# Kernel tuning notes

Hardware: AMD Instinct MI355X
Metric: run time of the kernel (lower is better)

The kernel has to match this reference:

```python
import jax, jax.numpy as jnp
import numpy as np

# Window-batch of 16x16 windows from a U-Net stage
B, C, H, W = 128, 128, 16, 16
HEADS = 8
EQK, EV = 128, 512      # embed_dim_qk, embed_dim_v (embed_dim=512, ratio=4)
L = H * W               # tokens per window (stride=1)


def _conv3x3(x, w, b):
    # NCHW 3x3 conv, padding 1
    out = jax.lax.conv_general_dilated(x, w, (1, 1), ((1, 1), (1, 1)),
                                       dimension_numbers=('NCHW', 'OIHW', 'NCHW'))
    return out + b[None, :, None, None]


def _pos_att(q, wq, bq, wk, bk, wv, bv, wo, bo, gamma):
    # MultiHeadAttention2D_POS, stride=1 -> conv_q/k/v are 1x1 convs
    hd, hdv = EQK // HEADS, EV // HEADS

    def proj(x, w, bias, d):
        y = jnp.einsum('bchw,ec->behw', x, w) + bias[None, :, None, None]
        return y.reshape(B, HEADS, d, L).transpose(0, 1, 3, 2)  # (B,h,L,d)

    pq = proj(q, wq, bq, hd)
    pk = proj(q, wk, bk, hd)
    pv = proj(q, wv, bv, hdv)
    attn = jax.nn.softmax(jnp.einsum('bhqd,bhkd->bhqk', pq, pk) * hd ** -0.5, axis=-1)
    out = jnp.einsum('bhqk,bhkd->bhqd', attn, pv)
    out = out.transpose(0, 1, 3, 2).reshape(B, EV, H, W)
    out = _conv3x3(out, wo, bo)             # proj_out: 3x3 conv EV->C
    return q + out * gamma                  # gamma-scaled residual


def _cha_att(q, wq, bq, wk, bk, wv, bv, wo, bo, gamma):
    # MultiHeadAttention2D_CHA: depthwise 1x1 grouped convs (channel multiplier = HEADS),
    # attention over the CHANNEL axis. Faithfully reproduces torch's reshape of the
    # group-major (c*HEADS+h) channel layout into (B, heads, C, L).
    def dwproj(x, w, bias):
        y = (x[:, :, None] * w.reshape(C, HEADS)[None, :, :, None, None]
             + bias.reshape(C, HEADS)[None, :, :, None, None])
        return y.reshape(B, C * HEADS, H, W).reshape(B, HEADS, C, L)

    pq = dwproj(q, wq, bq)
    pk = dwproj(q, wk, bk)
    pv = dwproj(q, wv, bv)
    attn = jax.nn.softmax(jnp.einsum('bhcl,bhdl->bhcd', pq, pk) * L ** -0.5, axis=-1)
    out = jnp.einsum('bhcd,bhdl->bhcl', attn, pv)      # (B,h,C,L)
    out = out.reshape(B, HEADS * C, H, W)
    # proj_out: grouped 1x1 ConvTranspose (== grouped 1x1 conv): sum each HEADS-sized group
    out = (out.reshape(B, C, HEADS, H, W)
           * wo.reshape(C, HEADS)[None, :, :, None, None]).sum(2) + bo[None, :, None, None]
    return q + out * gamma


def _forward(qkv_pos, qkv_cha,
             pos_wq, pos_bq, pos_wk, pos_bk, pos_wv, pos_bv, pos_wo, pos_bo, gamma_pos,
             cha_wq, cha_bq, cha_wk, cha_bk, cha_wv, cha_bv, cha_wo, cha_bo, gamma_cha,
             fuse_w, fuse_b):
    out_pos = _pos_att(qkv_pos, pos_wq, pos_bq, pos_wk, pos_bk, pos_wv, pos_bv,
                       pos_wo, pos_bo, gamma_pos)
    out_cha = _cha_att(qkv_cha, cha_wq, cha_bq, cha_wk, cha_bk, cha_wv, cha_bv,
                       cha_wo, cha_bo, gamma_cha)
    out = (out_pos + out_cha) * 0.5          # att_fusion='add' (slides=0 -> full slices)
    return _conv3x3(out, fuse_w, fuse_b)     # conv_out (Dropout2d is identity at eval)


def setup_inputs() -> dict:
    key = jax.random.key(0)
    ks = jax.random.split(key, 24)
    n = lambda k, shape, s=0.05: jax.random.normal(k, shape, dtype=jnp.float32) * s
    return {
        'qkv_pos': jax.random.normal(ks[0], (B, C, H, W), jnp.float32),
        'qkv_cha': jax.random.normal(ks[1], (B, C, H, W), jnp.float32),
        'pos_wq': n(ks[2], (EQK, C)), 'pos_bq': n(ks[3], (EQK,)),
        'pos_wk': n(ks[4], (EQK, C)), 'pos_bk': n(ks[5], (EQK,)),
        'pos_wv': n(ks[6], (EV, C)), 'pos_bv': n(ks[7], (EV,)),
        'pos_wo': n(ks[8], (C, EV, 3, 3)), 'pos_bo': n(ks[9], (C,)),
        'gamma_pos': jnp.array(0.1, jnp.float32),
        'cha_wq': n(ks[10], (C * HEADS,)), 'cha_bq': n(ks[11], (C * HEADS,)),
        'cha_wk': n(ks[12], (C * HEADS,)), 'cha_bk': n(ks[13], (C * HEADS,)),
        'cha_wv': n(ks[14], (C * HEADS,)), 'cha_bv': n(ks[15], (C * HEADS,)),
        'cha_wo': n(ks[16], (C * HEADS,)), 'cha_bo': n(ks[17], (C,)),
        'gamma_cha': jnp.array(0.1, jnp.float32),
        'fuse_w': n(ks[18], (C, C, 3, 3)), 'fuse_b': n(ks[19], (C,)),
    }


def reference(qkv_pos, qkv_cha,
              pos_wq, pos_bq, pos_wk, pos_bk, pos_wv, pos_bv, pos_wo, pos_bo, gamma_pos,
              cha_wq, cha_bq, cha_wk, cha_bk, cha_wv, cha_bv, cha_wo, cha_bo, gamma_cha,
              fuse_w, fuse_b):
    return _forward(qkv_pos, qkv_cha,
                    pos_wq, pos_bq, pos_wk, pos_bk, pos_wv, pos_bv, pos_wo, pos_bo, gamma_pos,
                    cha_wq, cha_bq, cha_wk, cha_bk, cha_wv, cha_bv, cha_wo, cha_bo, gamma_cha,
                    fuse_w, fuse_b)
```

## Files before the change

### kernel.cpp

```cpp
#include <hip/hip_runtime.h>
#include <cstdint>
#include <cstddef>

typedef unsigned short ushort_t;
typedef unsigned int uint_t;
typedef __attribute__((ext_vector_type(8))) short bf16x8;
typedef __attribute__((ext_vector_type(4))) float f32x4;

#define NB 128
#define NC 128
#define NL 256
#define NH 8
#define HD 16
#define HDV 64
#define NEV 512
#define PHALF 4194304

__device__ __forceinline__ ushort_t f2bf(float f) {
    uint_t u = __float_as_uint(f);
    u += 0x7fffu + ((u >> 16) & 1u);
    return (ushort_t)(u >> 16);
}
__device__ __forceinline__ float bf2f(ushort_t s) {
    return __uint_as_float(((uint_t)s) << 16);
}
__device__ __forceinline__ uint_t pack2(float lo, float hi) {
    uint_t r;
    asm("v_cvt_pk_bf16_f32 %0, %1, %2" : "=v"(r) : "v"(lo), "v"(hi));
    return r;
}

template<int CIN>
__global__ __launch_bounds__(256) void k_wpack(const float* __restrict__ w,
                                               short* __restrict__ wp) {
    int idx = blockIdx.x * 256 + threadIdx.x;
    if (idx >= CIN * 1152) return;
    int j    = idx & 7;
    int lane = (idx >> 3) & 63;
    int frag = idx >> 9;
    int rt   = frag & 7;
    int tap  = (frag >> 3) % 9;
    int ch   = frag / 72;
    int co   = rt * 16 + (lane & 15);
    int g    = lane >> 4;
    int ci   = ch * 32 + g * 8 + j;
    wp[idx] = (short)f2bf(w[((size_t)co * CIN + ci) * 9 + tap]);
}

template<int E>
__global__ __launch_bounds__(256) void k_wpack_qkv(const float* __restrict__ w,
                                                   short* __restrict__ wp) {
    int idx = blockIdx.x * 256 + threadIdx.x;
    if (idx >= E * 128) return;
    int j    = idx & 7;
    int lane = (idx >> 3) & 63;
    int ch   = (idx >> 9) & 3;
    int rt   = idx >> 11;
    int n = lane & 15, g = lane >> 4;
    wp[idx] = (short)f2bf(w[(size_t)(rt*16 + n)*128 + ch*32 + g*8 + j]);
}

__global__ __launch_bounds__(256) void k_xpose(const float* __restrict__ x,
                                               ushort_t* __restrict__ xbf) {
    const int half = blockIdx.x, b = blockIdx.y, t = threadIdx.x;
    const float* src = x + (size_t)b*NC*NL + (size_t)half*64*NL + t;
    uint_t* dst = (uint_t*)(xbf + ((size_t)b*NL + t)*NC + half*64);
    #pragma unroll
    for (int k8 = 0; k8 < 8; ++k8) {
        uint4 u;
        u.x = pack2(src[(k8*8+0)*NL], src[(k8*8+1)*NL]);
        u.y = pack2(src[(k8*8+2)*NL], src[(k8*8+3)*NL]);
        u.z = pack2(src[(k8*8+4)*NL], src[(k8*8+5)*NL]);
        u.w = pack2(src[(k8*8+6)*NL], src[(k8*8+7)*NL]);
        *(uint4*)(dst + k8*4) = u;
    }
}

__global__ __launch_bounds__(512, 4) void k_pos_mfma(
    const ushort_t* __restrict__ xbf,
    const short* __restrict__ wpq, const short* __restrict__ wpk,
    const short* __restrict__ wpv,
    const float* __restrict__ bq, const float* __restrict__ bk,
    const float* __restrict__ bv,
    ushort_t* __restrict__ att)
{
    const int h = blockIdx.x, b = blockIdx.y;
    const int t = threadIdx.x;
    const int lane = t & 63, w = t >> 6;
    const int n = lane & 15, g = lane >> 4;

    __shared__ __align__(16) short lds[26112];

    const f32x4 z4 = {0.f, 0.f, 0.f, 0.f};
    f32x4 qacc[2], kacc[2], vacc[4][2];
    #pragma unroll
    for (int ct = 0; ct < 2; ++ct) { qacc[ct] = z4; kacc[ct] = z4; }
    #pragma unroll
    for (int vt = 0; vt < 4; ++vt)
        #pragma unroll
        for (int ct = 0; ct < 2; ++ct) vacc[vt][ct] = z4;

    const ushort_t* xr = xbf + ((size_t)(b*NL + w*32 + n))*NC;

    #pragma unroll 2
    for (int ch = 0; ch < 4; ++ch) {
        bf16x8 xb[2];
        #pragma unroll
        for (int ct = 0; ct < 2; ++ct)
            xb[ct] = *(const bf16x8*)(xr + ct*16*NC + ch*32 + g*8);
        const size_t fo = ((size_t)((h*4 + ch)*64) + lane) * 8;
        {
            bf16x8 aq = *(const bf16x8*)(wpq + fo);
            #pragma unroll
            for (int ct = 0; ct < 2; ++ct)
                qacc[ct] = __builtin_amdgcn_mfma_f32_16x16x32_bf16(aq, xb[ct], qacc[ct], 0, 0, 0);
        }
        {
            bf16x8 ak = *(const bf16x8*)(wpk + fo);
            #pragma unroll
            for (int ct = 0; ct < 2; ++ct)
                kacc[ct] = __builtin_amdgcn_mfma_f32_16x16x32_bf16(ak, xb[ct], kacc[ct], 0, 0, 0);
        }
        #pragma unroll
        for (int vt = 0; vt < 4; ++vt) {
            bf16x8 av = *(const bf16x8*)(wpv + ((size_t)((((h*4 + vt)*4) + ch)*64) + lane) * 8);
            #pragma unroll
            for (int ct = 0; ct < 2; ++ct)
                vacc[vt][ct] = __builtin_amdgcn_mfma_f32_16x16x32_bf16(xb[ct], av, vacc[vt][ct], 0, 0, 0);
        }
    }

    uint_t qu01[2], qu23[2];
    {
        float bqv[4], bkv[4];
        #pragma unroll
        for (int r = 0; r < 4; ++r) {
            bqv[r] = bq[h*16 + g*4 + r];
            bkv[r] = bk[h*16 + g*4 + r];
        }
        #pragma unroll
        for (int ct = 0; ct < 2; ++ct) {
            qu01[ct] = pack2(qacc[ct][0] + bqv[0], qacc[ct][1] + bqv[1]);
            qu23[ct] = pack2(qacc[ct][2] + bqv[2], qacc[ct][3] + bqv[3]);
            uint2 kp;
            kp.x = pack2(kacc[ct][0] + bkv[0], kacc[ct][1] + bkv[1]);
            kp.y = pack2(kacc[ct][2] + bkv[2], kacc[ct][3] + bkv[3]);
            *(uint2*)&lds[(w*32 + ct*16 + n)*16 + g*4] = kp;
        }
        #pragma unroll
        for (int vt = 0; vt < 4; ++vt) {
            const float bvv = bv[h*64 + vt*16 + n];
            #pragma unroll
            for (int ct = 0; ct < 2; ++ct) {
                uint2 vp;
                vp.x = pack2(vacc[vt][ct][0] + bvv, vacc[vt][ct][1] + bvv);
                vp.y = pack2(vacc[vt][ct][2] + bvv, vacc[vt][ct][3] + bvv);
                *(uint2*)&lds[9216 + (vt*16 + n)*264 + w*32 + ct*16 + g*4] = vp;
            }
        }
    }
    __syncthreads();

    const int a0 = (n + 32*(g & 1)) * 4;
    #pragma unroll 1
    for (int qt = 0; qt < 2; ++qt) {
        union { uint_t u[4]; bf16x8 v; } qfu;
        qfu.u[0] = (uint_t)__builtin_amdgcn_ds_bpermute(a0,      (int)qu01[qt]);
        qfu.u[1] = (uint_t)__builtin_amdgcn_ds_bpermute(a0,      (int)qu23[qt]);
        qfu.u[2] = (uint_t)__builtin_amdgcn_ds_bpermute(a0 + 64, (int)qu01[qt]);
        qfu.u[3] = (uint_t)__builtin_amdgcn_ds_bpermute(a0 + 64, (int)qu23[qt]);
        if (g >= 2) { qfu.u[0] = 0; qfu.u[1] = 0; qfu.u[2] = 0; qfu.u[3] = 0; }
        bf16x8 qf = qfu.v;

        f32x4 s[16];
        #pragma unroll
        for (int kt = 0; kt < 16; ++kt) {
            bf16x8 kf = (bf16x8){0,0,0,0,0,0,0,0};
            if (g < 2) kf = *(const bf16x8*)&lds[(kt*16 + n)*16 + g*8];
            s[kt] = __builtin_amdgcn_mfma_f32_16x16x32_bf16(kf, qf, z4, 0, 0, 0);
        }
        float d0 = 0.f, d1 = 0.f, d2 = 0.f, d3 = 0.f;
        #pragma unroll
        for (int kt = 0; kt < 16; ++kt) {
            float e0 = exp2f(s[kt][0] * 0.36067376022224085f);
            float e1 = exp2f(s[kt][1] * 0.36067376022224085f);
            float e2 = exp2f(s[kt][2] * 0.36067376022224085f);
            float e3 = exp2f(s[kt][3] * 0.36067376022224085f);
            s[kt][0] = e0; s[kt][1] = e1; s[kt][2] = e2; s[kt][3] = e3;
            d0 += e0; d1 += e1; d2 += e2; d3 += e3;
        }
        float den = (d0 + d1) + (d2 + d3);
        den += __shfl_xor(den, 16);
        den += __shfl_xor(den, 32);
        const float inv = 1.f / den;

        f32x4 oacc[4] = {z4, z4, z4, z4};
        #pragma unroll
        for (int c2 = 0; c2 < 8; ++c2) {
            #pragma unroll
            for (int u = 0; u < 2; ++u) {
                const int kt = 2*c2 + u;
                uint2 pp;
                pp.x = pack2(s[kt][0], s[kt][1]);
                pp.y = pack2(s[kt][2], s[kt][3]);
                *(uint2*)&lds[4096 + w*640 + n*40 + u*16 + g*4] = pp;
            }
            bf16x8 pf = *(const bf16x8*)&lds[4096 + w*640 + n*40 + g*8];
            #pragma unroll
            for (int vt = 0; vt < 4; ++vt) {
                bf16x8 av = *(const bf16x8*)&lds[9216 + (vt*16 + n)*264 + c2*32 + g*8];
                oacc[vt] = __builtin_amdgcn_mfma_f32_16x16x32_bf16(av, pf, oacc[vt], 0, 0, 0);
            }
        }
        ushort_t* ap = att + (((size_t)b*NL + (w*32 + qt*16 + n))*NEV + h*HDV + g*4);
        #pragma unroll
        for (int vt = 0; vt < 4; ++vt) {
            uint2 op;
            op.x = pack2(oacc[vt][0]*inv, oacc[vt][1]*inv);
            op.y = pack2(oacc[vt][2]*inv, oacc[vt][3]*inv);
            *(uint2*)(ap + vt*16) = op;
        }
    }
}

__global__ __launch_bounds__(256, 1) void k_conv_ci(
    const ushort_t* __restrict__ att, const short* __restrict__ wp,
    ushort_t* __restrict__ P)
{
    const int kc = blockIdx.x, b = blockIdx.y;
    const int t = threadIdx.x;
    const int lane = t & 63, w = t >> 6;
    const int wr = w >> 1, wc = w & 1;
    const int n = lane & 15, gl = lane >> 4;

    __shared__ __align__(16) short ims[2][10368];

    {
        bf16x8 z = {0,0,0,0,0,0,0,0};
        bf16x8* p = (bf16x8*)&ims[0][0];
        for (int i = t; i < 2592; i += 256) p[i] = z;
    }

    f32x4 acc[4][8];
    #pragma unroll
    for (int i = 0; i < 4; ++i)
        #pragma unroll
        for (int j = 0; j < 8; ++j) acc[i][j] = (f32x4){0.f,0.f,0.f,0.f};

    const ushort_t* abase = att + (size_t)b*NL*NEV + kc*256;
    int soff[4], slots[4];
    #pragma unroll
    for (int i = 0; i < 4; ++i) {
        int id = t + 256*i;
        int gg = id & 3, xx = (id >> 2) & 15, yy = id >> 6;
        soff[i]  = (yy*16 + xx)*NEV + gg*8;
        slots[i] = (((yy+1)*4 + gg)*18 + xx + 1) * 8;
    }

    bf16x8 pre[4];
    #pragma unroll
    for (int i = 0; i < 4; ++i) pre[i] = *(const bf16x8*)(abase + soff[i]);
    __syncthreads();

    const int ybase = wc * 8;
    #pragma unroll 1
    for (int ch = 0; ch < 8; ++ch) {
        short* buf = &ims[ch & 1][0];
        #pragma unroll
        for (int i = 0; i < 4; ++i) *(bf16x8*)&buf[slots[i]] = pre[i];
        if (ch < 7) {
            #pragma unroll
            for (int i = 0; i < 4; ++i)
                pre[i] = *(const bf16x8*)(abase + soff[i] + (ch + 1)*32);
        }
        __syncthreads();
        #pragma unroll
        for (int dx = 0; dx < 3; ++dx) {
            bf16x8 Brow[10];
            #pragma unroll
            for (int r = 0; r < 10; ++r)
                Brow[r] = *(const bf16x8*)&buf[(((ybase + r)*4 + gl)*18 + n + dx) * 8];
            #pragma unroll
            for (int dy = 0; dy < 3; ++dy) {
                bf16x8 Af[4];
                #pragma unroll
                for (int rt = 0; rt < 4; ++rt)
                    Af[rt] = *(const bf16x8*)(wp +
                        ((size_t)(((kc*8 + ch)*9 + dy*3 + dx)*8 + wr*4 + rt)) * 512 + lane*8);
                #pragma unroll
                for (int ct = 0; ct < 8; ++ct)
                    #pragma unroll
                    for (int rt = 0; rt < 4; ++rt)
                        acc[rt][ct] = __builtin_amdgcn_mfma_f32_16x16x32_bf16(
                            Af[rt], Brow[ct + dy], acc[rt][ct], 0, 0, 0);
            }
        }
    }

    ushort_t* Pb = P + (size_t)kc * PHALF + (size_t)b * NL * NC;
    #pragma unroll
    for (int rt = 0; rt < 4; ++rt) {
        const int co0 = wr*64 + rt*16 + gl*4;
        #pragma unroll
        for (int ct = 0; ct < 8; ++ct) {
            const int l = wc*128 + ct*16 + n;
            uint2 u;
            u.x = pack2(acc[rt][ct][0], acc[rt][ct][1]);
            u.y = pack2(acc[rt][ct][2], acc[rt][ct][3]);
            *(uint2*)(Pb + (size_t)l*NC + co0) = u;
        }
    }
}

__global__ __launch_bounds__(256, 1) void k_conv_co(
    const float* __restrict__ comb, const short* __restrict__ wp,
    const float* __restrict__ bias, float* __restrict__ out)
{
    const int coh = blockIdx.x, b = blockIdx.y;
    const int t = threadIdx.x;
    const int lane = t & 63, w = t >> 6;
    const int wr = w >> 1, wc = w & 1;
    const int n = lane & 15, gl = lane >> 4;

    __shared__ __align__(16) short ims[2][10368];

    {
        bf16x8 z = {0,0,0,0,0,0,0,0};
        bf16x8* p = (bf16x8*)&ims[0][0];
        for (int i = t; i < 2592; i += 256) p[i] = z;
    }

    f32x4 acc[2][8];
    #pragma unroll
    for (int i = 0; i < 2; ++i)
        #pragma unroll
        for (int j = 0; j < 8; ++j) acc[i][j] = (f32x4){0.f,0.f,0.f,0.f};

    const float* cbase = comb + (size_t)b*NL*NC;
    int soff[4], slots[4];
    #pragma unroll
    for (int i = 0; i < 4; ++i) {
        int id = t + 256*i;
        int gg = id & 3, xx = (id >> 2) & 15, yy = id >> 6;
        soff[i]  = (yy*16 + xx)*NC + gg*8;
        slots[i] = (((yy+1)*4 + gg)*18 + xx + 1) * 8;
    }

    float4 pa[4], pb[4];
    #pragma unroll
    for (int i = 0; i < 4; ++i) {
        pa[i] = *(const float4*)(cbase + soff[i]);
        pb[i] = *(const float4*)(cbase + soff[i] + 4);
    }
    __syncthreads();

    const int ybase = wc * 8;
    #pragma unroll 1
    for (int ch = 0; ch < 4; ++ch) {
        short* buf = &ims[ch & 1][0];
        #pragma unroll
        for (int i = 0; i < 4; ++i) {
            uint4 u;
            u.x = pack2(pa[i].x, pa[i].y);  u.y = pack2(pa[i].z, pa[i].w);
            u.z = pack2(pb[i].x, pb[i].y);  u.w = pack2(pb[i].z, pb[i].w);
            *(uint4*)&buf[slots[i]] = u;
        }
        if (ch < 3) {
            #pragma unroll
            for (int i = 0; i < 4; ++i) {
                pa[i] = *(const float4*)(cbase + soff[i] + (ch + 1)*32);
                pb[i] = *(const float4*)(cbase + soff[i] + (ch + 1)*32 + 4);
            }
        }
        __syncthreads();
        #pragma unroll
        for (int dx = 0; dx < 3; ++dx) {
            bf16x8 Brow[10];
            #pragma unroll
            for (int r = 0; r < 10; ++r)
                Brow[r] = *(const bf16x8*)&buf[(((ybase + r)*4 + gl)*18 + n + dx) * 8];
            #pragma unroll
            for (int dy = 0; dy < 3; ++dy) {
                bf16x8 Af[2];
                #pragma unroll
                for (int rt = 0; rt < 2; ++rt)
                    Af[rt] = *(const bf16x8*)(wp +
                        ((size_t)((ch*9 + dy*3 + dx)*8 + coh*4 + wr*2 + rt)) * 512 + lane*8);
                #pragma unroll
                for (int ct = 0; ct < 8; ++ct)
                    #pragma unroll
                    for (int rt = 0; rt < 2; ++rt)
                        acc[rt][ct] = __builtin_amdgcn_mfma_f32_16x16x32_bf16(
                            Af[rt], Brow[ct + dy], acc[rt][ct], 0, 0, 0);
            }
        }
    }

    #pragma unroll
    for (int rt = 0; rt < 2; ++rt) {
        const int co0 = coh*64 + wr*32 + rt*16 + gl*4;
        const float c0 = bias[co0+0], c1 = bias[co0+1],
                    c2 = bias[co0+2], c3 = bias[co0+3];
        #pragma unroll
        for (int ct = 0; ct < 8; ++ct) {
            const int l = wc*128 + ct*16 + n;
            f32x4 a = acc[rt][ct];
            out[((size_t)b*NC + co0+0)*NL + l] = c0 + a[0];
            out[((size_t)b*NC + co0+1)*NL + l] = c1 + a[1];
            out[((size_t)b*NC + co0+2)*NL + l] = c2 + a[2];
            out[((size_t)b*NC + co0+3)*NL + l] = c3 + a[3];
        }
    }
}

#define NLP 260
__global__ __launch_bounds__(256) void k_cha(
    const float* __restrict__ xc,
    const float* __restrict__ cwq, const float* __restrict__ cbq,
    const float* __restrict__ cwk, const float* __restrict__ cbk,
    const float* __restrict__ cwv, const float* __restrict__ cbv,
    const float* __restrict__ cwo, const float* __restrict__ cbo,
    const float* __restrict__ gamma,
    const ushort_t* __restrict__ P, const float* __restrict__ qpos,
    const float* __restrict__ pbo, const float* __restrict__ gpos,
    float* __restrict__ comb)
{
    const int h = blockIdx.x, b = blockIdx.y, t = threadIdx.x;
    __shared__ float qh[16][NLP];
    __shared__ float G_s[16][17];
    __shared__ float S_s[16];
    __shared__ float wq_s[128], bq_s[128], wk_s[128], bk_s[128], wv_s[128], bv_s[128];
    __shared__ float A_s[128][17];
    __shared__ float B_s[128];
    __shared__ float M_s[16][17];
    __shared__ float c_s[16];

    #pragma unroll
    for (int j = 0; j < 16; ++j)
        qh[j][t] = xc[((size_t)b*NC + h*16 + j)*NL + t];
    if (t < 128) {
        const int k = h*128 + t;
        wq_s[t] = cwq[k]; bq_s[t] = cbq[k];
        wk_s[t] = cwk[k]; bk_s[t] = cbk[k];
        wv_s[t] = cwv[k]; bv_s[t] = cbv[k];
    }
    __syncthreads();
    {
        const int i = t >> 4, j = t & 15;
        const float4* qi = (const float4*)qh[i];
        const float4* qj = (const float4*)qh[j];
        float gg = 0.f;
        for (int l4 = 0; l4 < NL/4; ++l4) {
            float4 a = qi[l4], c = qj[l4];
            gg = fmaf(a.x,c.x,fmaf(a.y,c.y,fmaf(a.z,c.z,fmaf(a.w,c.w,gg))));
        }
        G_s[i][j] = gg;
    }
    if (t < 16) {
        const float4* qi = (const float4*)qh[t];
        float s = 0.f;
        for (int l4 = 0; l4 < NL/4; ++l4) { float4 a = qi[l4]; s += a.x + a.y + a.z + a.w; }
        S_s[t] = s;
    }
    __syncthreads();
    if (t < 128) {
        const int c2 = t, cg = c2 >> 3;
        const float wqc = wq_s[c2], bqc = bq_s[c2];
        float Pv[16];
        #pragma unroll
        for (int j = 0; j < 16; ++j) Pv[j] = wqc*G_s[cg][j] + bqc*S_s[j];
        const float Qc = wqc*S_s[cg] + bqc*256.0f;
        float mx = -3.0e38f;
        #pragma unroll
        for (int dg = 0; dg < 16; ++dg) {
            #pragma unroll
            for (int dj = 0; dj < 8; ++dj) {
                const int d = dg*8 + dj;
                float s = wk_s[d]*Pv[dg] + bk_s[d]*Qc;
                mx = fmaxf(mx, s);
            }
        }
        float A[16];
        #pragma unroll
        for (int j = 0; j < 16; ++j) A[j] = 0.f;
        float Bv = 0.f, den = 0.f;
        #pragma unroll
        for (int dg = 0; dg < 16; ++dg) {
            #pragma unroll
            for (int dj = 0; dj < 8; ++dj) {
                const int d = dg*8 + dj;
                float s = wk_s[d]*Pv[dg] + bk_s[d]*Qc;
                float e = __expf((s - mx) * 0.0625f);
                den += e;
                A[dg] = fmaf(e, wv_s[d], A[dg]);
                Bv = fmaf(e, bv_s[d], Bv);
            }
        }
        const float inv = 1.f / den;
        #pragma unroll
        for (int j = 0; j < 16; ++j) A_s[c2][j] = A[j]*inv;
        B_s[c2] = Bv*inv;
    }
    __syncthreads();
    {
        const int cl = t >> 4, j = t & 15;
        const int cp = h*16 + cl;
        float m = 0.f;
        #pragma unroll
        for (int hp = 0; hp < 8; ++hp)
            m = fmaf(cwo[cp*8+hp], A_s[cl*8+hp][j], m);
        M_s[cl][j] = m;
        if (j == 0) {
            float cc = cbo[cp];
            #pragma unroll
            for (int hp = 0; hp < 8; ++hp)
                cc = fmaf(cwo[cp*8+hp], B_s[cl*8+hp], cc);
            c_s[cl] = cc;
        }
    }
    __syncthreads();
    {
        const float g  = gamma[0];
        const float gp = gpos[0];
        const int l = t;
        float av[16];
        #pragma unroll
        for (int cl = 0; cl < 16; ++cl) {
            float a = c_s[cl];
            #pragma unroll
            for (int j = 0; j < 16; ++j)
                a = fmaf(M_s[cl][j], qh[j][l], a);
            av[cl] = a;
        }
        const ushort_t* p0 = P + ((size_t)b*NL + l)*NC + h*16;
        const ushort_t* p1 = p0 + PHALF;
        const float* qp = qpos + ((size_t)b*NC + h*16)*NL + l;
        float4* cp4 = (float4*)(comb + ((size_t)b*NL + l)*NC + h*16);
        #pragma unroll
        for (int q = 0; q < 4; ++q) {
            uint2 u0 = *(const uint2*)(p0 + 4*q);
            uint2 u1 = *(const uint2*)(p1 + 4*q);
            float s0 = bf2f((ushort_t)(u0.x & 0xffffu)) + bf2f((ushort_t)(u1.x & 0xffffu));
            float s1 = bf2f((ushort_t)(u0.x >> 16))     + bf2f((ushort_t)(u1.x >> 16));
            float s2 = bf2f((ushort_t)(u0.y & 0xffffu)) + bf2f((ushort_t)(u1.y & 0xffffu));
            float s3 = bf2f((ushort_t)(u0.y >> 16))     + bf2f((ushort_t)(u1.y >> 16));
            float4 c;
            c.x = 0.5f*(qp[(4*q+0)*NL] + gp*(pbo[h*16+4*q+0] + s0) + qh[4*q+0][l] + g*av[4*q+0]);
            c.y = 0.5f*(qp[(4*q+1)*NL] + gp*(pbo[h*16+4*q+1] + s1) + qh[4*q+1][l] + g*av[4*q+1]);
            c.z = 0.5f*(qp[(4*q+2)*NL] + gp*(pbo[h*16+4*q+2] + s2) + qh[4*q+2][l] + g*av[4*q+2]);
            c.w = 0.5f*(qp[(4*q+3)*NL] + gp*(pbo[h*16+4*q+3] + s3) + qh[4*q+3][l] + g*av[4*q+3]);
            cp4[q] = c;
        }
    }
}

extern "C" void kernel_launch(void* const* d_in, const int* in_sizes, int n_in,
                              void* d_out, int out_size, void* d_ws, size_t ws_size,
                              hipStream_t stream)
{
    const float* qpos = (const float*)d_in[0];
    const float* qcha = (const float*)d_in[1];
    const float* pwq  = (const float*)d_in[2];
    const float* pbq  = (const float*)d_in[3];
    const float* pwk  = (const float*)d_in[4];
    const float* pbk  = (const float*)d_in[5];
    const float* pwv  = (const float*)d_in[6];
    const float* pbv  = (const float*)d_in[7];
    const float* pwo  = (const float*)d_in[8];
    const float* pbo  = (const float*)d_in[9];
    const float* gpos = (const float*)d_in[10];
    const float* cwq  = (const float*)d_in[11];
    const float* cbq  = (const float*)d_in[12];
    const float* cwk  = (const float*)d_in[13];
    const float* cbk  = (const float*)d_in[14];
    const float* cwv  = (const float*)d_in[15];
    const float* cbv  = (const float*)d_in[16];
    const float* cwo  = (const float*)d_in[17];
    const float* cbo  = (const float*)d_in[18];
    const float* gcha = (const float*)d_in[19];
    const float* fw   = (const float*)d_in[20];
    const float* fb   = (const float*)d_in[21];
    float* outp = (float*)d_out;

    char* ws = (char*)d_ws;
    ushort_t* att  = (ushort_t*)ws;
    float*    comb = (float*)ws;
    ushort_t* P    = (ushort_t*)(ws + 33554432);
    ushort_t* xbf  = (ushort_t*)(ws + 33554432);
    short*    wp1  = (short*)(ws + 50331648);
    short*    wp2  = (short*)(ws + 51511296);
    short*    wpq  = (short*)(ws + 51806208);
    short*    wpk  = (short*)(ws + 51838976);
    short*    wpv  = (short*)(ws + 51871744);

    k_wpack<NEV><<<dim3((NEV*1152 + 255)/256), 256, 0, stream>>>(pwo, wp1);
    k_wpack<NC ><<<dim3((NC *1152 + 255)/256), 256, 0, stream>>>(fw,  wp2);
    k_wpack_qkv<128><<<dim3(64),  256, 0, stream>>>(pwq, wpq);
    k_wpack_qkv<128><<<dim3(64),  256, 0, stream>>>(pwk, wpk);
    k_wpack_qkv<512><<<dim3(256), 256, 0, stream>>>(pwv, wpv);

    k_xpose<<<dim3(2, NB), 256, 0, stream>>>(qpos, xbf);
    k_pos_mfma<<<dim3(NH, NB), 512, 0, stream>>>(xbf, wpq, wpk, wpv,
                                                 pbq, pbk, pbv, att);
    k_conv_ci<<<dim3(2, NB), 256, 0, stream>>>(att, wp1, P);
    k_cha<<<dim3(NH, NB), 256, 0, stream>>>(qcha, cwq, cbq, cwk, cbk, cwv, cbv,
                                            cwo, cbo, gcha,
                                            P, qpos, pbo, gpos, comb);
    k_conv_co<<<dim3(2, NB), 256, 0, stream>>>(comb, wp2, fb, outp);
}
```

Baseline: 178.4 us.

## Drop LDS im2col staging in 3x3 convs, load B fragments directly from global

Both 3x3 conv kernels stop staging a padded image in LDS and instead gather B fragments straight from global memory with boundary masking. Each block now covers half (or a quarter) of the spatial tile, which doubles the grid and raises the occupancy hint to 4 blocks per CU. The weight pack layout is reordered so each lane reads four contiguous A fragments per tap. The combined intermediate is stored as bf16 instead of fp32, halving that round trip. In exchange the kernels re-read overlapping activations from global/L2 per tap, and precision of the fuse-conv input drops.

Measured after the change: 283.9 us. +59.2%, slower.

```diff
diff --git a/kernel.cpp b/kernel.cpp
--- a/kernel.cpp
+++ b/kernel.cpp
@@ -36,14 +36,14 @@
     int idx = blockIdx.x * 256 + threadIdx.x;
     if (idx >= CIN * 1152) return;
     int j    = idx & 7;
-    int lane = (idx >> 3) & 63;
-    int frag = idx >> 9;
-    int rt   = frag & 7;
-    int tap  = (frag >> 3) % 9;
-    int ch   = frag / 72;
-    int co   = rt * 16 + (lane & 15);
-    int g    = lane >> 4;
-    int ci   = ch * 32 + g * 8 + j;
+    int r    = (idx >> 3) & 3;
+    int lane = (idx >> 5) & 63;
+    int gidx = (idx >> 11) & 1;
+    int tc   = idx >> 12;
+    int tap  = tc % 9;
+    int ch   = tc / 9;
+    int co   = (gidx * 4 + r) * 16 + (lane & 15);
+    int ci   = ch * 32 + (lane >> 4) * 8 + j;
     wp[idx] = (short)f2bf(w[((size_t)co * CIN + ci) * 9 + tap]);
 }
 
@@ -223,76 +223,55 @@
     }
 }
 
-__global__ __launch_bounds__(256, 1) void k_conv_ci(
+__global__ __launch_bounds__(256, 4) void k_conv_ci(
     const ushort_t* __restrict__ att, const short* __restrict__ wp,
     ushort_t* __restrict__ P)
 {
-    const int kc = blockIdx.x, b = blockIdx.y;
+    const int kc = blockIdx.x >> 1, lh = blockIdx.x & 1, b = blockIdx.y;
     const int t = threadIdx.x;
     const int lane = t & 63, w = t >> 6;
     const int wr = w >> 1, wc = w & 1;
     const int n = lane & 15, gl = lane >> 4;
-
-    __shared__ __align__(16) short ims[2][10368];
-
-    {
-        bf16x8 z = {0,0,0,0,0,0,0,0};
-        bf16x8* p = (bf16x8*)&ims[0][0];
-        for (int i = t; i < 2592; i += 256) p[i] = z;
-    }
-
-    f32x4 acc[4][8];
+    const int ybase = lh*8 + wc*4;
+
+    f32x4 acc[4][4];
     #pragma unroll
     for (int i = 0; i < 4; ++i)
         #pragma unroll
-        for (int j = 0; j < 8; ++j) acc[i][j] = (f32x4){0.f,0.f,0.f,0.f};
-
-    const ushort_t* abase = att + (size_t)b*NL*NEV + kc*256;
-    int soff[4], slots[4];
-    #pragma unroll
-    for (int i = 0; i < 4; ++i) {
-        int id = t + 256*i;
-        int gg = id & 3, xx = (id >> 2) & 15, yy = id >> 6;
-        soff[i]  = (yy*16 + xx)*NEV + gg*8;
-        slots[i] = (((yy+1)*4 + gg)*18 + xx + 1) * 8;
-    }
-
-    bf16x8 pre[4];
-    #pragma unroll
-    for (int i = 0; i < 4; ++i) pre[i] = *(const bf16x8*)(abase + soff[i]);
-    __syncthreads();
-
-    const int ybase = wc * 8;
+        for (int j = 0; j < 4; ++j) acc[i][j] = (f32x4){0.f,0.f,0.f,0.f};
+
+    const short* wpl = wp + (size_t)lane * 32;
+    const ushort_t* abase = att + (size_t)b*NL*NEV + kc*256 + gl*8;
+    const bf16x8 zf = {0,0,0,0,0,0,0,0};
+
     #pragma unroll 1
     for (int ch = 0; ch < 8; ++ch) {
-        short* buf = &ims[ch & 1][0];
-        #pragma unroll
-        for (int i = 0; i < 4; ++i) *(bf16x8*)&buf[slots[i]] = pre[i];
-        if (ch < 7) {
-            #pragma unroll
-            for (int i = 0; i < 4; ++i)
-                pre[i] = *(const bf16x8*)(abase + soff[i] + (ch + 1)*32);
-        }
-        __syncthreads();
-        #pragma unroll
-        for (int dx = 0; dx < 3; ++dx) {
-            bf16x8 Brow[10];
-            #pragma unroll
-            for (int r = 0; r < 10; ++r)
-                Brow[r] = *(const bf16x8*)&buf[(((ybase + r)*4 + gl)*18 + n + dx) * 8];
-            #pragma unroll
-            for (int dy = 0; dy < 3; ++dy) {
-                bf16x8 Af[4];
-                #pragma unroll
-                for (int rt = 0; rt < 4; ++rt)
-                    Af[rt] = *(const bf16x8*)(wp +
-                        ((size_t)(((kc*8 + ch)*9 + dy*3 + dx)*8 + wr*4 + rt)) * 512 + lane*8);
-                #pragma unroll
-                for (int ct = 0; ct < 8; ++ct)
-                    #pragma unroll
-                    for (int rt = 0; rt < 4; ++rt)
-                        acc[rt][ct] = __builtin_amdgcn_mfma_f32_16x16x32_bf16(
-                            Af[rt], Brow[ct + dy], acc[rt][ct], 0, 0, 0);
+        const int ch16 = kc*8 + ch;
+        #pragma unroll
+        for (int tap = 0; tap < 9; ++tap) {
+            const int dy = tap / 3, dx = tap % 3;
+            const int x = n + dx - 1;
+            const bool xok = (x >= 0) && (x < 16);
+            bf16x8 Bf[4];
+            #pragma unroll
+            for (int ct = 0; ct < 4; ++ct) {
+                Bf[ct] = zf;
+                const int row = ybase + ct + dy - 1;
+                if (row >= 0 && row < 16) {
+                    if (xok)
+                        Bf[ct] = *(const bf16x8*)(abase +
+                            ((size_t)(row*16 + x))*NEV + ch*32);
+                }
+            }
+            const bf16x8* ap = (const bf16x8*)(wpl +
+                ((size_t)((ch16*9 + tap)*2 + wr)) * 2048);
+            bf16x8 Af0 = ap[0], Af1 = ap[1], Af2 = ap[2], Af3 = ap[3];
+            #pragma unroll
+            for (int ct = 0; ct < 4; ++ct) {
+                acc[0][ct] = __builtin_amdgcn_mfma_f32_16x16x32_bf16(Af0, Bf[ct], acc[0][ct], 0, 0, 0);
+                acc[1][ct] = __builtin_amdgcn_mfma_f32_16x16x32_bf16(Af1, Bf[ct], acc[1][ct], 0, 0, 0);
+                acc[2][ct] = __builtin_amdgcn_mfma_f32_16x16x32_bf16(Af2, Bf[ct], acc[2][ct], 0, 0, 0);
+                acc[3][ct] = __builtin_amdgcn_mfma_f32_16x16x32_bf16(Af3, Bf[ct], acc[3][ct], 0, 0, 0);
             }
         }
     }
@@ -302,8 +281,8 @@
     for (int rt = 0; rt < 4; ++rt) {
         const int co0 = wr*64 + rt*16 + gl*4;
         #pragma unroll
-        for (int ct = 0; ct < 8; ++ct) {
-            const int l = wc*128 + ct*16 + n;
+        for (int ct = 0; ct < 4; ++ct) {
+            const int l = lh*128 + wc*64 + ct*16 + n;
             uint2 u;
             u.x = pack2(acc[rt][ct][0], acc[rt][ct][1]);
             u.y = pack2(acc[rt][ct][2], acc[rt][ct][3]);
@@ -312,98 +291,67 @@
     }
 }
 
-__global__ __launch_bounds__(256, 1) void k_conv_co(
-    const float* __restrict__ comb, const short* __restrict__ wp,
+__global__ __launch_bounds__(256, 4) void k_conv_co(
+    const ushort_t* __restrict__ comb, const short* __restrict__ wp,
     const float* __restrict__ bias, float* __restrict__ out)
 {
-    const int coh = blockIdx.x, b = blockIdx.y;
+    const int lq = blockIdx.x, b = blockIdx.y;
     const int t = threadIdx.x;
     const int lane = t & 63, w = t >> 6;
     const int wr = w >> 1, wc = w & 1;
     const int n = lane & 15, gl = lane >> 4;
-
-    __shared__ __align__(16) short ims[2][10368];
-
-    {
-        bf16x8 z = {0,0,0,0,0,0,0,0};
-        bf16x8* p = (bf16x8*)&ims[0][0];
-        for (int i = t; i < 2592; i += 256) p[i] = z;
-    }
-
-    f32x4 acc[2][8];
-    #pragma unroll
-    for (int i = 0; i < 2; ++i)
-        #pragma unroll
-        for (int j = 0; j < 8; ++j) acc[i][j] = (f32x4){0.f,0.f,0.f,0.f};
-
-    const float* cbase = comb + (size_t)b*NL*NC;
-    int soff[4], slots[4];
+    const int ybase = lq*4 + wc*2;
+
+    f32x4 acc[4][2];
     #pragma unroll
     for (int i = 0; i < 4; ++i) {
-        int id = t + 256*i;
-        int gg = id & 3, xx = (id >> 2) & 15, yy = id >> 6;
-        soff[i]  = (yy*16 + xx)*NC + gg*8;
-        slots[i] = (((yy+1)*4 + gg)*18 + xx + 1) * 8;
-    }
-
-    float4 pa[4], pb[4];
-    #pragma unroll
-    for (int i = 0; i < 4; ++i) {
-        pa[i] = *(const float4*)(cbase + soff[i]);
-        pb[i] = *(const float4*)(cbase + soff[i] + 4);
-    }
-    __syncthreads();
-
-    const int ybase = wc * 8;
+        acc[i][0] = (f32x4){0.f,0.f,0.f,0.f};
+        acc[i][1] = (f32x4){0.f,0.f,0.f,0.f};
+    }
+
+    const short* wpl = wp + (size_t)lane * 32;
+    const ushort_t* cbase = comb + (size_t)b*NL*NC + gl*8;
+    const bf16x8 zf = {0,0,0,0,0,0,0,0};
+
     #pragma unroll 1
     for (int ch = 0; ch < 4; ++ch) {
-        short* buf = &ims[ch & 1][0];
-        #pragma unroll
-        for (int i = 0; i < 4; ++i) {
-            uint4 u;
-            u.x = pack2(pa[i].x, pa[i].y);  u.y = pack2(pa[i].z, pa[i].w);
-            u.z = pack2(pb[i].x, pb[i].y);  u.w = pack2(pb[i].z, pb[i].w);
-            *(uint4*)&buf[slots[i]] = u;
-        }
-        if (ch < 3) {
-            #pragma unroll
-            for (int i = 0; i < 4; ++i) {
-                pa[i] = *(const float4*)(cbase + soff[i] + (ch + 1)*32);
-                pb[i] = *(const float4*)(cbase + soff[i] + (ch + 1)*32 + 4);
-            }
-        }
-        __syncthreads();
-        #pragma unroll
-        for (int dx = 0; dx < 3; ++dx) {
-            bf16x8 Brow[10];
-            #pragma unroll
-            for (int r = 0; r < 10; ++r)
-                Brow[r] = *(const bf16x8*)&buf[(((ybase + r)*4 + gl)*18 + n + dx) * 8];
-            #pragma unroll
-            for (int dy = 0; dy < 3; ++dy) {
-                bf16x8 Af[2];
-                #pragma unroll
-                for (int rt = 0; rt < 2; ++rt)
-                    Af[rt] = *(const bf16x8*)(wp +
-                        ((size_t)((ch*9 + dy*3 + dx)*8 + coh*4 + wr*2 + rt)) * 512 + lane*8);
-                #pragma unroll
-                for (int ct = 0; ct < 8; ++ct)
-                    #pragma unroll
-                    for (int rt = 0; rt < 2; ++rt)
-                        acc[rt][ct] = __builtin_amdgcn_mfma_f32_16x16x32_bf16(
-                            Af[rt], Brow[ct + dy], acc[rt][ct], 0, 0, 0);
-            }
-        }
-    }
-
-    #pragma unroll
-    for (int rt = 0; rt < 2; ++rt) {
-        const int co0 = coh*64 + wr*32 + rt*16 + gl*4;
+        #pragma unroll
+        for (int tap = 0; tap < 9; ++tap) {
+            const int dy = tap / 3, dx = tap % 3;
+            const int x = n + dx - 1;
+            const bool xok = (x >= 0) && (x < 16);
+            bf16x8 Bf[2];
+            #pragma unroll
+            for (int ct = 0; ct < 2; ++ct) {
+                Bf[ct] = zf;
+                const int row = ybase + ct + dy - 1;
+                if (row >= 0 && row < 16) {
+                    if (xok)
+                        Bf[ct] = *(const bf16x8*)(cbase +
+                            ((size_t)(row*16 + x))*NC + ch*32);
+                }
+            }
+            const bf16x8* ap = (const bf16x8*)(wpl +
+                ((size_t)((ch*9 + tap)*2 + wr)) * 2048);
+            bf16x8 Af0 = ap[0], Af1 = ap[1], Af2 = ap[2], Af3 = ap[3];
+            #pragma unroll
+            for (int ct = 0; ct < 2; ++ct) {
+                acc[0][ct] = __builtin_amdgcn_mfma_f32_16x16x32_bf16(Af0, Bf[ct], acc[0][ct], 0, 0, 0);
+                acc[1][ct] = __builtin_amdgcn_mfma_f32_16x16x32_bf16(Af1, Bf[ct], acc[1][ct], 0, 0, 0);
+                acc[2][ct] = __builtin_amdgcn_mfma_f32_16x16x32_bf16(Af2, Bf[ct], acc[2][ct], 0, 0, 0);
+                acc[3][ct] = __builtin_amdgcn_mfma_f32_16x16x32_bf16(Af3, Bf[ct], acc[3][ct], 0, 0, 0);
+            }
+        }
+    }
+
+    #pragma unroll
+    for (int rt = 0; rt < 4; ++rt) {
+        const int co0 = wr*64 + rt*16 + gl*4;
         const float c0 = bias[co0+0], c1 = bias[co0+1],
                     c2 = bias[co0+2], c3 = bias[co0+3];
         #pragma unroll
-        for (int ct = 0; ct < 8; ++ct) {
-            const int l = wc*128 + ct*16 + n;
+        for (int ct = 0; ct < 2; ++ct) {
+            const int l = lq*64 + wc*32 + ct*16 + n;
             f32x4 a = acc[rt][ct];
             out[((size_t)b*NC + co0+0)*NL + l] = c0 + a[0];
             out[((size_t)b*NC + co0+1)*NL + l] = c1 + a[1];
@@ -423,7 +371,7 @@
     const float* __restrict__ gamma,
     const ushort_t* __restrict__ P, const float* __restrict__ qpos,
     const float* __restrict__ pbo, const float* __restrict__ gpos,
-    float* __restrict__ comb)
+    ushort_t* __restrict__ comb)
 {
     const int h = blockIdx.x, b = blockIdx.y, t = threadIdx.x;
     __shared__ float qh[16][NLP];
@@ -523,19 +471,18 @@
         const float g  = gamma[0];
         const float gp = gpos[0];
         const int l = t;
-        float av[16];
+        float cv[16];
         #pragma unroll
         for (int cl = 0; cl < 16; ++cl) {
             float a = c_s[cl];
             #pragma unroll
             for (int j = 0; j < 16; ++j)
                 a = fmaf(M_s[cl][j], qh[j][l], a);
-            av[cl] = a;
+            cv[cl] = a;
         }
         const ushort_t* p0 = P + ((size_t)b*NL + l)*NC + h*16;
         const ushort_t* p1 = p0 + PHALF;
         const float* qp = qpos + ((size_t)b*NC + h*16)*NL + l;
-        float4* cp4 = (float4*)(comb + ((size_t)b*NL + l)*NC + h*16);
         #pragma unroll
         for (int q = 0; q < 4; ++q) {
             uint2 u0 = *(const uint2*)(p0 + 4*q);
@@ -544,13 +491,19 @@
             float s1 = bf2f((ushort_t)(u0.x >> 16))     + bf2f((ushort_t)(u1.x >> 16));
             float s2 = bf2f((ushort_t)(u0.y & 0xffffu)) + bf2f((ushort_t)(u1.y & 0xffffu));
             float s3 = bf2f((ushort_t)(u0.y >> 16))     + bf2f((ushort_t)(u1.y >> 16));
-            float4 c;
-            c.x = 0.5f*(qp[(4*q+0)*NL] + gp*(pbo[h*16+4*q+0] + s0) + qh[4*q+0][l] + g*av[4*q+0]);
-            c.y = 0.5f*(qp[(4*q+1)*NL] + gp*(pbo[h*16+4*q+1] + s1) + qh[4*q+1][l] + g*av[4*q+1]);
-            c.z = 0.5f*(qp[(4*q+2)*NL] + gp*(pbo[h*16+4*q+2] + s2) + qh[4*q+2][l] + g*av[4*q+2]);
-            c.w = 0.5f*(qp[(4*q+3)*NL] + gp*(pbo[h*16+4*q+3] + s3) + qh[4*q+3][l] + g*av[4*q+3]);
-            cp4[q] = c;
-        }
+            cv[4*q+0] = 0.5f*(qp[(4*q+0)*NL] + gp*(pbo[h*16+4*q+0] + s0) + qh[4*q+0][l] + g*cv[4*q+0]);
+            cv[4*q+1] = 0.5f*(qp[(4*q+1)*NL] + gp*(pbo[h*16+4*q+1] + s1) + qh[4*q+1][l] + g*cv[4*q+1]);
+            cv[4*q+2] = 0.5f*(qp[(4*q+2)*NL] + gp*(pbo[h*16+4*q+2] + s2) + qh[4*q+2][l] + g*cv[4*q+2]);
+            cv[4*q+3] = 0.5f*(qp[(4*q+3)*NL] + gp*(pbo[h*16+4*q+3] + s3) + qh[4*q+3][l] + g*cv[4*q+3]);
+        }
+        ushort_t* cp = comb + ((size_t)b*NL + l)*NC + h*16;
+        uint4 o0, o1;
+        o0.x = pack2(cv[0],  cv[1]);   o0.y = pack2(cv[2],  cv[3]);
+        o0.z = pack2(cv[4],  cv[5]);   o0.w = pack2(cv[6],  cv[7]);
+        o1.x = pack2(cv[8],  cv[9]);   o1.y = pack2(cv[10], cv[11]);
+        o1.z = pack2(cv[12], cv[13]);  o1.w = pack2(cv[14], cv[15]);
+        *(uint4*)cp       = o0;
+        *(uint4*)(cp + 8) = o1;
     }
 }
 
@@ -584,7 +537,7 @@
 
     char* ws = (char*)d_ws;
     ushort_t* att  = (ushort_t*)ws;
-    float*    comb = (float*)ws;
+    ushort_t* comb = (ushort_t*)ws;
     ushort_t* P    = (ushort_t*)(ws + 33554432);
     ushort_t* xbf  = (ushort_t*)(ws + 33554432);
     short*    wp1  = (short*)(ws + 50331648);
@@ -602,9 +555,9 @@
     k_xpose<<<dim3(2, NB), 256, 0, stream>>>(qpos, xbf);
     k_pos_mfma<<<dim3(NH, NB), 512, 0, stream>>>(xbf, wpq, wpk, wpv,
                                                  pbq, pbk, pbv, att);
-    k_conv_ci<<<dim3(2, NB), 256, 0, stream>>>(att, wp1, P);
+    k_conv_ci<<<dim3(4, NB), 256, 0, stream>>>(att, wp1, P);
     k_cha<<<dim3(NH, NB), 256, 0, stream>>>(qcha, cwq, cbq, cwk, cbk, cwv, cbv,
                                             cwo, cbo, gcha,
                                             P, qpos, pbo, gpos, comb);
-    k_conv_co<<<dim3(2, NB), 256, 0, stream>>>(comb, wp2, fb, outp);
-}
+    k_conv_co<<<dim3(4, NB), 256, 0, stream>>>(comb, wp2, fb, outp);
+}
```
